# Optimization experiments

Measured on AMD Instinct MI355X. Metric: run time of the kernel, lower is better.

## Reference

```python
import jax, jax.numpy as jnp
import numpy as np

T, B, N, D = 32, 8, 256, 512
TAU = 2.0   # LIF membrane time constant
VTH = 1.0   # spike threshold
ALPHA = 4.0 # surrogate-gradient sharpness


def setup_inputs() -> dict:
    key = jax.random.key(0)
    k0, k1, k2 = jax.random.split(key, 3)
    scale = 1.0 / np.sqrt(D)
    return {
        "x": jax.random.normal(k0, (T, B, N, D), jnp.float32),
        "tr_mx": jnp.zeros((B, N, D), jnp.float32),            # initial membrane state
        "W_lif": jax.random.normal(k1, (D, D), jnp.float32) * scale,
        "b_lif": jnp.zeros((D,), jnp.float32),
        "W_rec": jax.random.normal(k2, (D, D), jnp.float32) * scale,  # recon2 weight (d_ff=D -> patch_size=D)
        "b_rec": jnp.zeros((D,), jnp.float32),
    }


def _spike(v):
    # Heaviside forward, sigmoid surrogate backward (standard SNN straight-through)
    s = jax.nn.sigmoid(ALPHA * v)
    return s + jax.lax.stop_gradient((v > 0).astype(v.dtype) - s)


def reference(x, tr_mx, W_lif, b_lif, W_rec, b_rec):
    # MemoryUpdate.replay: tau-decayed LIF recurrence over time, emitting spike gate per step
    inp = jnp.einsum('tbnd,de->tbne', x, W_lif) + b_lif   # [T,B,N,D] input current

    def step(mem, i_t):
        mem = mem + (i_t - mem) / TAU        # leaky integration
        sp = _spike(mem - VTH)               # fire
        mem = mem * (1.0 - sp)               # hard reset
        return mem, sp

    _, sp_seq = jax.lax.scan(step, tr_mx, inp)  # sp_seq: [T,B,N,D]

    g = x * (1.0 - sp_seq)                       # gated residual
    rec_x = jnp.einsum('tbnd,dp->tbnp', g, W_rec) + b_rec  # recon2 on flattened (T*B, N, D)
    return rec_x
```

## Files before the change

### kernel.cpp

```cpp
#include <hip/hip_runtime.h>
#include <hip/hip_bf16.h>


#define TT 32
#define TH 16
#define CH 8
#define BB 8
#define NN 256
#define DD 512

typedef __attribute__((ext_vector_type(8))) short short8;
typedef __attribute__((ext_vector_type(4))) float f32x4;

__device__ __forceinline__ unsigned short f2bf(float f) {
    __hip_bfloat16 h = __float2bfloat16(f);
    return *reinterpret_cast<unsigned short*>(&h);
}

__global__ void cast_transpose_wr(const float* __restrict__ Wr,
                                  unsigned short* __restrict__ Wt) {
    int idx = blockIdx.x * 256 + threadIdx.x;
    int d = idx >> 9;
    int p = idx & 511;
    Wt[p * DD + d] = f2bf(Wr[idx]);
}

__global__ __launch_bounds__(128, 2) void lif_phaseA_g16(
    const float* __restrict__ x,
    const float* __restrict__ tr_mx,
    const float* __restrict__ Wl,
    const float* __restrict__ bl,
    unsigned short* __restrict__ gws)
{
    __shared__ __align__(16) float xs[TH * DD];

    const int tid = threadIdx.x;
    const int tok = blockIdx.x;
    const int e0  = tid * 4;
    const size_t base = (size_t)tok * DD;
    const size_t st   = (size_t)BB * NN * DD;

    float acc[TH][4];
    float m[4];
    {
        const float4 m4 = *reinterpret_cast<const float4*>(&tr_mx[base + e0]);
        m[0] = m4.x; m[1] = m4.y; m[2] = m4.z; m[3] = m4.w;
    }

    #pragma unroll 1
    for (int half = 0; half < 2; ++half) {
        #pragma unroll
        for (int r = 0; r < 16; ++r) {
            const int flat = r * 128 + tid;
            const int row  = flat >> 7;
            const int c4   = flat & 127;
            const float4 v = *reinterpret_cast<const float4*>(
                &x[(size_t)(half * TH + row) * st + base + c4 * 4]);
            *reinterpret_cast<float4*>(&xs[row * DD + c4 * 4]) = v;
        }
        __syncthreads();

        {
            const float4 blv = *reinterpret_cast<const float4*>(&bl[e0]);
            #pragma unroll
            for (int i = 0; i < TH; ++i) {
                acc[i][0] = blv.x; acc[i][1] = blv.y;
                acc[i][2] = blv.z; acc[i][3] = blv.w;
            }
        }

        #pragma unroll 2
        for (int d = 0; d < DD; d += 4) {
            const float4 w0 = *reinterpret_cast<const float4*>(&Wl[(size_t)(d + 0) * DD + e0]);
            const float4 w1 = *reinterpret_cast<const float4*>(&Wl[(size_t)(d + 1) * DD + e0]);
            const float4 w2 = *reinterpret_cast<const float4*>(&Wl[(size_t)(d + 2) * DD + e0]);
            const float4 w3 = *reinterpret_cast<const float4*>(&Wl[(size_t)(d + 3) * DD + e0]);
            #pragma unroll
            for (int i = 0; i < TH; ++i) {
                const float4 xv = *reinterpret_cast<const float4*>(&xs[i * DD + d]);
                acc[i][0] = fmaf(xv.x, w0.x, acc[i][0]);
                acc[i][1] = fmaf(xv.x, w0.y, acc[i][1]);
                acc[i][2] = fmaf(xv.x, w0.z, acc[i][2]);
                acc[i][3] = fmaf(xv.x, w0.w, acc[i][3]);
                acc[i][0] = fmaf(xv.y, w1.x, acc[i][0]);
                acc[i][1] = fmaf(xv.y, w1.y, acc[i][1]);
                acc[i][2] = fmaf(xv.y, w1.z, acc[i][2]);
                acc[i][3] = fmaf(xv.y, w1.w, acc[i][3]);
                acc[i][0] = fmaf(xv.z, w2.x, acc[i][0]);
                acc[i][1] = fmaf(xv.z, w2.y, acc[i][1]);
                acc[i][2] = fmaf(xv.z, w2.z, acc[i][2]);
                acc[i][3] = fmaf(xv.z, w2.w, acc[i][3]);
                acc[i][0] = fmaf(xv.w, w3.x, acc[i][0]);
                acc[i][1] = fmaf(xv.w, w3.y, acc[i][1]);
                acc[i][2] = fmaf(xv.w, w3.z, acc[i][2]);
                acc[i][3] = fmaf(xv.w, w3.w, acc[i][3]);
            }
        }

        #pragma unroll
        for (int i = 0; i < TH; ++i) {
            const int t = half * TH + i;
            const float4 xv = *reinterpret_cast<const float4*>(&xs[i * DD + e0]);
            const float xr[4] = {xv.x, xv.y, xv.z, xv.w};
            float g[4];
            #pragma unroll
            for (int e = 0; e < 4; ++e) {
                m[e] = m[e] + (acc[i][e] - m[e]) * 0.5f;
                const float s = (m[e] - 1.0f > 0.0f) ? 1.0f : 0.0f;
                g[e] = (s > 0.0f) ? 0.0f : xr[e];
                m[e] *= (1.0f - s);
            }
            uint2 p;
            p.x = (unsigned)f2bf(g[0]) | ((unsigned)f2bf(g[1]) << 16);
            p.y = (unsigned)f2bf(g[2]) | ((unsigned)f2bf(g[3]) << 16);
            *reinterpret_cast<uint2*>(&gws[((size_t)tok * TT + t) * DD + e0]) = p;
        }
        __syncthreads();
    }
}

__global__ __launch_bounds__(512, 2) void lif_phaseB4(
    const unsigned short* __restrict__ gws,
    const unsigned short* __restrict__ Wt,
    const float* __restrict__ br,
    float* __restrict__ out)
{
    const int tid = threadIdx.x;
    const int w    = tid >> 6;
    const int lane = tid & 63;
    const int hB   = w & 1;
    const int q    = w >> 1;
    const int lcol = lane & 15;
    const int lkg  = lane >> 4;
    const int tA   = hB * 16 + lcol;
    const size_t st = (size_t)BB * NN * DD;
    const int colb = q * 128;
    const int tok0 = blockIdx.x * 2;

    const unsigned short* arow0 = &gws[((size_t)tok0 * TT + tA) * DD];
    const unsigned short* arow1 = &gws[((size_t)(tok0 + 1) * TT + tA) * DD];

    f32x4 acc0[8], acc1[8];
    #pragma unroll
    for (int nt = 0; nt < 8; ++nt) {
        const float b = br[colb + nt * 16 + lcol];
        acc0[nt] = (f32x4){b, b, b, b};
        acc1[nt] = (f32x4){b, b, b, b};
    }

    #pragma unroll 1
    for (int ks = 0; ks < 16; ++ks) {
        const int kb = ks * 32 + lkg * 8;
        const short8 a0 = *reinterpret_cast<const short8*>(&arow0[kb]);
        const short8 a1 = *reinterpret_cast<const short8*>(&arow1[kb]);
        #pragma unroll
        for (int nt = 0; nt < 8; ++nt) {
            const int col = colb + nt * 16 + lcol;
            const short8 bf = *reinterpret_cast<const short8*>(&Wt[(size_t)col * DD + kb]);
            acc0[nt] = __builtin_amdgcn_mfma_f32_16x16x32_bf16(a0, bf, acc0[nt], 0, 0, 0);
            acc1[nt] = __builtin_amdgcn_mfma_f32_16x16x32_bf16(a1, bf, acc1[nt], 0, 0, 0);
        }
    }

    #pragma unroll
    for (int nt = 0; nt < 8; ++nt) {
        const int col = colb + nt * 16 + lcol;
        #pragma unroll
        for (int r = 0; r < 4; ++r) {
            const int t = hB * 16 + lkg * 4 + r;
            out[(size_t)t * st + (size_t)tok0 * DD + col]       = acc0[nt][r];
            out[(size_t)t * st + (size_t)(tok0 + 1) * DD + col] = acc1[nt][r];
        }
    }
}

__global__ __launch_bounds__(128, 4) void lif_phaseA_m(
    const float* __restrict__ x, const float* __restrict__ tr_mx,
    const float* __restrict__ Wl, const float* __restrict__ bl,
    unsigned* __restrict__ gmsk)
{
    __shared__ __align__(16) float xs[CH * 256];

    const int tid = threadIdx.x;
    const int tok = blockIdx.x;
    const int e0  = tid * 4;
    const size_t base = (size_t)tok * DD;
    const size_t st   = (size_t)BB * NN * DD;

    float acc[CH][4];
    float4 m4 = *reinterpret_cast<const float4*>(&tr_mx[base + e0]);
    float m[4] = {m4.x, m4.y, m4.z, m4.w};
    unsigned mc[4] = {0u, 0u, 0u, 0u};
    const float4 blv = *reinterpret_cast<const float4*>(&bl[e0]);
    const float blr[4] = {blv.x, blv.y, blv.z, blv.w};

    #pragma unroll 1
    for (int tg = 0; tg < 4; ++tg) {
        #pragma unroll
        for (int i = 0; i < CH; ++i)
            #pragma unroll
            for (int e = 0; e < 4; ++e) acc[i][e] = blr[e];

        #pragma unroll 1
        for (int h = 0; h < 2; ++h) {
            #pragma unroll
            for (int r = 0; r < 4; ++r) {
                const int flat = r * 128 + tid;
                const int row  = flat >> 6;
                const int c4   = flat & 63;
                const float4 v = *reinterpret_cast<const float4*>(
                    &x[(size_t)(tg * CH + row) * st + base + h * 256 + c4 * 4]);
                *reinterpret_cast<float4*>(&xs[row * 256 + c4 * 4]) = v;
            }
            __syncthreads();

            #pragma unroll 2
            for (int dd_ = 0; dd_ < 256; dd_ += 4) {
                const int d = h * 256 + dd_;
                const float4 w0 = *reinterpret_cast<const float4*>(&Wl[(size_t)(d + 0) * DD + e0]);
                const float4 w1 = *reinterpret_cast<const float4*>(&Wl[(size_t)(d + 1) * DD + e0]);
                const float4 w2 = *reinterpret_cast<const float4*>(&Wl[(size_t)(d + 2) * DD + e0]);
                const float4 w3 = *reinterpret_cast<const float4*>(&Wl[(size_t)(d + 3) * DD + e0]);
                #pragma unroll
                for (int i = 0; i < CH; ++i) {
                    const float4 xv = *reinterpret_cast<const float4*>(&xs[i * 256 + dd_]);
                    acc[i][0] = fmaf(xv.x, w0.x, acc[i][0]);
                    acc[i][1] = fmaf(xv.x, w0.y, acc[i][1]);
                    acc[i][2] = fmaf(xv.x, w0.z, acc[i][2]);
                    acc[i][3] = fmaf(xv.x, w0.w, acc[i][3]);
                    acc[i][0] = fmaf(xv.y, w1.x, acc[i][0]);
                    acc[i][1] = fmaf(xv.y, w1.y, acc[i][1]);
                    acc[i][2] = fmaf(xv.y, w1.z, acc[i][2]);
                    acc[i][3] = fmaf(xv.y, w1.w, acc[i][3]);
                    acc[i][0] = fmaf(xv.z, w2.x, acc[i][0]);
                    acc[i][1] = fmaf(xv.z, w2.y, acc[i][1]);
                    acc[i][2] = fmaf(xv.z, w2.z, acc[i][2]);
                    acc[i][3] = fmaf(xv.z, w2.w, acc[i][3]);
                    acc[i][0] = fmaf(xv.w, w3.x, acc[i][0]);
                    acc[i][1] = fmaf(xv.w, w3.y, acc[i][1]);
                    acc[i][2] = fmaf(xv.w, w3.z, acc[i][2]);
                    acc[i][3] = fmaf(xv.w, w3.w, acc[i][3]);
                }
            }
            __syncthreads();
        }

        #pragma unroll
        for (int i = 0; i < CH; ++i) {
            const int t = tg * CH + i;
            #pragma unroll
            for (int e = 0; e < 4; ++e) {
                m[e] = m[e] + (acc[i][e] - m[e]) * 0.5f;
                const float s = (m[e] - 1.0f > 0.0f) ? 1.0f : 0.0f;
                mc[e] |= (s > 0.0f) ? (1u << t) : 0u;
                m[e] *= (1.0f - s);
            }
        }
    }

    uint4 mv;
    mv.x = mc[0]; mv.y = mc[1]; mv.z = mc[2]; mv.w = mc[3];
    *reinterpret_cast<uint4*>(&gmsk[base + e0]) = mv;
}

template<bool UW>
__global__ __launch_bounds__(256, 2) void lif_phaseB2(
    const float* __restrict__ x, const float* __restrict__ Wr,
    const float* __restrict__ br, const unsigned short* __restrict__ Wt,
    const unsigned* __restrict__ gmsk, float* __restrict__ out)
{
    __shared__ __align__(16) unsigned ms[2 * DD];

    const int tid = threadIdx.x;
    const size_t st = (size_t)BB * NN * DD;
    {
        const uint4 v = *reinterpret_cast<const uint4*>(
            &gmsk[(size_t)blockIdx.x * 2 * DD + tid * 4]);
        *reinterpret_cast<uint4*>(&ms[tid * 4]) = v;
    }
    __syncthreads();

    const int wv   = tid >> 6;
    const int lane = tid & 63;
    const int qB   = wv >> 1;
    const int hB   = wv & 1;
    const int lcol = lane & 15;
    const int lkg  = lane >> 4;
    const int tA   = hB * 16 + lcol;
    const size_t baseB = (size_t)(blockIdx.x * 2 + qB) * DD;
    const unsigned* mq = &ms[qB * DD];
    const float* xrow = &x[(size_t)tA * st + baseB];

    #pragma unroll 1
    for (int pass = 0; pass < 4; ++pass) {
        const int colb = pass * 128;
        f32x4 acc[8];
        #pragma unroll
        for (int nt = 0; nt < 8; ++nt) {
            const float b = br[colb + nt * 16 + lcol];
            acc[nt] = (f32x4){b, b, b, b};
        }
        #pragma unroll 1
        for (int ks = 0; ks < 16; ++ks) {
            const int kb = ks * 32 + lkg * 8;
            const float4 x0 = *reinterpret_cast<const float4*>(&xrow[kb]);
            const float4 x1 = *reinterpret_cast<const float4*>(&xrow[kb + 4]);
            const uint4 m0 = *reinterpret_cast<const uint4*>(&mq[kb]);
            const uint4 m1 = *reinterpret_cast<const uint4*>(&mq[kb + 4]);
            short8 a;
            a[0] = (short)f2bf(((m0.x >> tA) & 1u) ? 0.0f : x0.x);
            a[1] = (short)f2bf(((m0.y >> tA) & 1u) ? 0.0f : x0.y);
            a[2] = (short)f2bf(((m0.z >> tA) & 1u) ? 0.0f : x0.z);
            a[3] = (short)f2bf(((m0.w >> tA) & 1u) ? 0.0f : x0.w);
            a[4] = (short)f2bf(((m1.x >> tA) & 1u) ? 0.0f : x1.x);
            a[5] = (short)f2bf(((m1.y >> tA) & 1u) ? 0.0f : x1.y);
            a[6] = (short)f2bf(((m1.z >> tA) & 1u) ? 0.0f : x1.z);
            a[7] = (short)f2bf(((m1.w >> tA) & 1u) ? 0.0f : x1.w);
            #pragma unroll
            for (int nt = 0; nt < 8; ++nt) {
                const int col = colb + nt * 16 + lcol;
                short8 bf;
                if (UW) {
                    bf = *reinterpret_cast<const short8*>(&Wt[(size_t)col * DD + kb]);
                } else {
                    #pragma unroll
                    for (int j = 0; j < 8; ++j)
                        bf[j] = (short)f2bf(Wr[(size_t)(kb + j) * DD + col]);
                }
                acc[nt] = __builtin_amdgcn_mfma_f32_16x16x32_bf16(a, bf, acc[nt], 0, 0, 0);
            }
        }
        #pragma unroll
        for (int nt = 0; nt < 8; ++nt) {
            const int col = colb + nt * 16 + lcol;
            #pragma unroll
            for (int r = 0; r < 4; ++r) {
                const int t = hB * 16 + lkg * 4 + r;
                out[(size_t)t * st + baseB + col] = acc[nt][r];
            }
        }
    }
}

extern "C" void kernel_launch(void* const* d_in, const int* in_sizes, int n_in,
                              void* d_out, int out_size, void* d_ws, size_t ws_size,
                              hipStream_t stream) {
    const float* x     = (const float*)d_in[0];
    const float* tr_mx = (const float*)d_in[1];
    const float* Wl    = (const float*)d_in[2];
    const float* bl    = (const float*)d_in[3];
    const float* Wr    = (const float*)d_in[4];
    const float* br    = (const float*)d_in[5];
    float* out = (float*)d_out;

    const size_t g_bytes   = (size_t)BB * NN * TT * DD * 2;
    const size_t wt_bytes  = (size_t)DD * DD * 2;
    const size_t msk_bytes = (size_t)BB * NN * DD * 4;

    if (ws_size >= g_bytes + wt_bytes) {
        unsigned short* gws = (unsigned short*)d_ws;
        unsigned short* Wt  = (unsigned short*)((char*)d_ws + g_bytes);
        cast_transpose_wr<<<dim3(1024), dim3(256), 0, stream>>>(Wr, Wt);
        lif_phaseA_g16<<<dim3(BB * NN), dim3(128), 0, stream>>>(x, tr_mx, Wl, bl, gws);
        lif_phaseB4<<<dim3(BB * NN / 2), dim3(512), 0, stream>>>(gws, Wt, br, out);
    } else if (ws_size >= msk_bytes + wt_bytes) {
        unsigned* gmsk = (unsigned*)d_ws;
        unsigned short* Wt = (unsigned short*)((char*)d_ws + msk_bytes);
        cast_transpose_wr<<<dim3(1024), dim3(256), 0, stream>>>(Wr, Wt);
        lif_phaseA_m<<<dim3(BB * NN), dim3(128), 0, stream>>>(x, tr_mx, Wl, bl, gmsk);
        lif_phaseB2<true><<<dim3(BB * NN / 2), dim3(256), 0, stream>>>(x, Wr, br, Wt, gmsk, out);
    } else if (ws_size >= msk_bytes) {
        unsigned* gmsk = (unsigned*)d_ws;
        lif_phaseA_m<<<dim3(BB * NN), dim3(128), 0, stream>>>(x, tr_mx, Wl, bl, gmsk);
        lif_phaseB2<false><<<dim3(BB * NN / 2), dim3(256), 0, stream>>>(x, Wr, br, nullptr, gmsk, out);
    }
}
```

Before: 699.8 us.

## Process two tokens per block in phase A with split-K x staging

Phase A now runs 256-thread blocks that each handle two tokens, so every W_lif row load is shared by twice as many threads. The x tile in shared memory is staged in two halves along the reduction dimension, which keeps the LDS footprint at 32KB per block. The gating epilogue re-reads x from global memory because the staged tile no longer holds full rows. This trades extra global reads and more barriers for fewer blocks and better weight reuse through the cache.

```diff
diff --git a/kernel.cpp b/kernel.cpp
--- a/kernel.cpp
+++ b/kernel.cpp
@@ -25,18 +25,20 @@
     Wt[p * DD + d] = f2bf(Wr[idx]);
 }
 
-__global__ __launch_bounds__(128, 2) void lif_phaseA_g16(
+__global__ __launch_bounds__(256, 2) void lif_phaseA_e4t16(
     const float* __restrict__ x,
     const float* __restrict__ tr_mx,
     const float* __restrict__ Wl,
     const float* __restrict__ bl,
     unsigned short* __restrict__ gws)
 {
-    __shared__ __align__(16) float xs[TH * DD];
+    __shared__ __align__(16) float xs[2 * TH * 256];
 
     const int tid = threadIdx.x;
-    const int tok = blockIdx.x;
-    const int e0  = tid * 4;
+    const int tq  = tid >> 7;
+    const int tl  = tid & 127;
+    const int e0  = tl * 4;
+    const int tok = blockIdx.x * 2 + tq;
     const size_t base = (size_t)tok * DD;
     const size_t st   = (size_t)BB * NN * DD;
 
@@ -48,18 +50,7 @@
     }
 
     #pragma unroll 1
-    for (int half = 0; half < 2; ++half) {
-        #pragma unroll
-        for (int r = 0; r < 16; ++r) {
-            const int flat = r * 128 + tid;
-            const int row  = flat >> 7;
-            const int c4   = flat & 127;
-            const float4 v = *reinterpret_cast<const float4*>(
-                &x[(size_t)(half * TH + row) * st + base + c4 * 4]);
-            *reinterpret_cast<float4*>(&xs[row * DD + c4 * 4]) = v;
-        }
-        __syncthreads();
-
+    for (int ht = 0; ht < 2; ++ht) {
         {
             const float4 blv = *reinterpret_cast<const float4*>(&bl[e0]);
             #pragma unroll
@@ -69,38 +60,59 @@
             }
         }
 
-        #pragma unroll 2
-        for (int d = 0; d < DD; d += 4) {
-            const float4 w0 = *reinterpret_cast<const float4*>(&Wl[(size_t)(d + 0) * DD + e0]);
-            const float4 w1 = *reinterpret_cast<const float4*>(&Wl[(size_t)(d + 1) * DD + e0]);
-            const float4 w2 = *reinterpret_cast<const float4*>(&Wl[(size_t)(d + 2) * DD + e0]);
-            const float4 w3 = *reinterpret_cast<const float4*>(&Wl[(size_t)(d + 3) * DD + e0]);
-            #pragma unroll
-            for (int i = 0; i < TH; ++i) {
-                const float4 xv = *reinterpret_cast<const float4*>(&xs[i * DD + d]);
-                acc[i][0] = fmaf(xv.x, w0.x, acc[i][0]);
-                acc[i][1] = fmaf(xv.x, w0.y, acc[i][1]);
-                acc[i][2] = fmaf(xv.x, w0.z, acc[i][2]);
-                acc[i][3] = fmaf(xv.x, w0.w, acc[i][3]);
-                acc[i][0] = fmaf(xv.y, w1.x, acc[i][0]);
-                acc[i][1] = fmaf(xv.y, w1.y, acc[i][1]);
-                acc[i][2] = fmaf(xv.y, w1.z, acc[i][2]);
-                acc[i][3] = fmaf(xv.y, w1.w, acc[i][3]);
-                acc[i][0] = fmaf(xv.z, w2.x, acc[i][0]);
-                acc[i][1] = fmaf(xv.z, w2.y, acc[i][1]);
-                acc[i][2] = fmaf(xv.z, w2.z, acc[i][2]);
-                acc[i][3] = fmaf(xv.z, w2.w, acc[i][3]);
-                acc[i][0] = fmaf(xv.w, w3.x, acc[i][0]);
-                acc[i][1] = fmaf(xv.w, w3.y, acc[i][1]);
-                acc[i][2] = fmaf(xv.w, w3.z, acc[i][2]);
-                acc[i][3] = fmaf(xv.w, w3.w, acc[i][3]);
-            }
+        #pragma unroll 1
+        for (int hd = 0; hd < 2; ++hd) {
+            #pragma unroll
+            for (int r = 0; r < 8; ++r) {
+                const int flat = r * 256 + tid;
+                const int q    = flat >> 10;
+                const int rem  = flat & 1023;
+                const int row  = rem >> 6;
+                const int c4   = rem & 63;
+                const float4 v = *reinterpret_cast<const float4*>(
+                    &x[(size_t)(ht * TH + row) * st
+                       + (size_t)(blockIdx.x * 2 + q) * DD + hd * 256 + c4 * 4]);
+                *reinterpret_cast<float4*>(&xs[(q * TH + row) * 256 + c4 * 4]) = v;
+            }
+            __syncthreads();
+
+            const float* xsl = &xs[tq * TH * 256];
+
+            #pragma unroll 2
+            for (int dd_ = 0; dd_ < 256; dd_ += 4) {
+                const int d = hd * 256 + dd_;
+                const float4 w0 = *reinterpret_cast<const float4*>(&Wl[(size_t)(d + 0) * DD + e0]);
+                const float4 w1 = *reinterpret_cast<const float4*>(&Wl[(size_t)(d + 1) * DD + e0]);
+                const float4 w2 = *reinterpret_cast<const float4*>(&Wl[(size_t)(d + 2) * DD + e0]);
+                const float4 w3 = *reinterpret_cast<const float4*>(&Wl[(size_t)(d + 3) * DD + e0]);
+                #pragma unroll
+                for (int i = 0; i < TH; ++i) {
+                    const float4 xv = *reinterpret_cast<const float4*>(&xsl[i * 256 + dd_]);
+                    acc[i][0] = fmaf(xv.x, w0.x, acc[i][0]);
+                    acc[i][1] = fmaf(xv.x, w0.y, acc[i][1]);
+                    acc[i][2] = fmaf(xv.x, w0.z, acc[i][2]);
+                    acc[i][3] = fmaf(xv.x, w0.w, acc[i][3]);
+                    acc[i][0] = fmaf(xv.y, w1.x, acc[i][0]);
+                    acc[i][1] = fmaf(xv.y, w1.y, acc[i][1]);
+                    acc[i][2] = fmaf(xv.y, w1.z, acc[i][2]);
+                    acc[i][3] = fmaf(xv.y, w1.w, acc[i][3]);
+                    acc[i][0] = fmaf(xv.z, w2.x, acc[i][0]);
+                    acc[i][1] = fmaf(xv.z, w2.y, acc[i][1]);
+                    acc[i][2] = fmaf(xv.z, w2.z, acc[i][2]);
+                    acc[i][3] = fmaf(xv.z, w2.w, acc[i][3]);
+                    acc[i][0] = fmaf(xv.w, w3.x, acc[i][0]);
+                    acc[i][1] = fmaf(xv.w, w3.y, acc[i][1]);
+                    acc[i][2] = fmaf(xv.w, w3.z, acc[i][2]);
+                    acc[i][3] = fmaf(xv.w, w3.w, acc[i][3]);
+                }
+            }
+            __syncthreads();
         }
 
         #pragma unroll
         for (int i = 0; i < TH; ++i) {
-            const int t = half * TH + i;
-            const float4 xv = *reinterpret_cast<const float4*>(&xs[i * DD + e0]);
+            const int t = ht * TH + i;
+            const float4 xv = *reinterpret_cast<const float4*>(&x[(size_t)t * st + base + e0]);
             const float xr[4] = {xv.x, xv.y, xv.z, xv.w};
             float g[4];
             #pragma unroll
@@ -115,7 +127,6 @@
             p.y = (unsigned)f2bf(g[2]) | ((unsigned)f2bf(g[3]) << 16);
             *reinterpret_cast<uint2*>(&gws[((size_t)tok * TT + t) * DD + e0]) = p;
         }
-        __syncthreads();
     }
 }
 
@@ -361,7 +372,7 @@
         unsigned short* gws = (unsigned short*)d_ws;
         unsigned short* Wt  = (unsigned short*)((char*)d_ws + g_bytes);
         cast_transpose_wr<<<dim3(1024), dim3(256), 0, stream>>>(Wr, Wt);
-        lif_phaseA_g16<<<dim3(BB * NN), dim3(128), 0, stream>>>(x, tr_mx, Wl, bl, gws);
+        lif_phaseA_e4t16<<<dim3(BB * NN / 2), dim3(256), 0, stream>>>(x, tr_mx, Wl, bl, gws);
         lif_phaseB4<<<dim3(BB * NN / 2), dim3(512), 0, stream>>>(gws, Wt, br, out);
     } else if (ws_size >= msk_bytes + wt_bytes) {
         unsigned* gmsk = (unsigned*)d_ws;
```

Result: slower. 717.2 us (+2.5%).
